# Kernel optimization log

Measured on AMD Instinct MI355X. Metric: run time of the kernel, lower is better.

The kernel has to match this reference:

```python
import jax, jax.numpy as jnp
import numpy as np

N_NODES = 50000
N_EDGES = 800000
NUM_FEAT = 100
F_DIM = 64
R_ROUNDS = 4
L_FP = 128
NUM_CLASS = 10


def setup_inputs() -> dict:
    key = jax.random.key(0)
    ks = jax.random.split(key, 10)
    s = 0.05
    return {
        "node_feature": jax.random.randint(ks[0], (N_NODES,), 0, NUM_FEAT),
        "edge_src": jax.random.randint(ks[1], (N_EDGES,), 0, N_NODES),
        "edge_dst": jax.random.randint(ks[2], (N_EDGES,), 0, N_NODES),
        "emb_table": jax.random.normal(ks[3], (NUM_FEAT, F_DIM), jnp.float32) * s,
        "W_h": jax.random.normal(ks[4], (R_ROUNDS, F_DIM, F_DIM), jnp.float32) * s,
        "b_h": jax.random.normal(ks[5], (R_ROUNDS, F_DIM), jnp.float32) * s,
        "W_fp": jax.random.normal(ks[6], (R_ROUNDS, F_DIM, L_FP), jnp.float32) * s,
        "b_fp": jax.random.normal(ks[7], (R_ROUNDS, L_FP), jnp.float32) * s,
        "W_cl": jax.random.normal(ks[8], (L_FP, NUM_CLASS), jnp.float32) * s,
        "b_cl": jax.random.normal(ks[9], (NUM_CLASS,), jnp.float32) * s,
    }


def reference(node_feature, edge_src, edge_dst, emb_table, W_h, b_h, W_fp, b_fp, W_cl, b_cl):
    # Initial node embeddings: [N, F]
    emb = emb_table[node_feature]
    f = jnp.zeros((L_FP,), dtype=emb.dtype)
    for r_i in range(R_ROUNDS):
        # v[node] = emb[node] + sum_{nbr in neighbours(node)} emb[nbr]
        agg = jax.ops.segment_sum(emb[edge_src], edge_dst, num_segments=N_NODES)
        v = emb + agg
        # per-node tiny MLP, batched over all nodes
        r = jax.nn.relu(v @ W_h[r_i] + b_h[r_i])            # [N, F]
        i = jax.nn.softmax(r @ W_fp[r_i] + b_fp[r_i], axis=-1)  # [N, L]
        f = f + i.sum(axis=0)                                # accumulate fingerprint
        emb = r                                              # synchronous update
    return jax.nn.softmax(f @ W_cl + b_cl, axis=-1)
```

## Files before the change

### kernel.cpp

```cpp
#include <hip/hip_runtime.h>
#include <hip/hip_bf16.h>

#define FDIM 64
#define LFP 128
#define RROUNDS 4
#define BM 64
#define PCHUNK 4096
#define CB 512
#define MAXB 10240
#define RSL 32

typedef __attribute__((ext_vector_type(8))) short bf16x8;
typedef __attribute__((ext_vector_type(4))) float f32x4;

__device__ __forceinline__ float bf2f(unsigned short u) {
    unsigned int x = ((unsigned int)u) << 16;
    float f;
    __builtin_memcpy(&f, &x, 4);
    return f;
}
__device__ __forceinline__ unsigned short f2bf(float x) {
    unsigned int u;
    __builtin_memcpy(&u, &x, 4);
    unsigned int r = (u + 0x7fffu + ((u >> 16) & 1u)) >> 16;
    return (unsigned short)r;
}

__global__ __launch_bounds__(256) void chist_kernel(const int* __restrict__ dst,
                                                    int* __restrict__ chist, int nE, int nbc) {
    __shared__ int scnt[128];
    int t = threadIdx.x;
    if (t < 128) scnt[t] = 0;
    __syncthreads();
    int c0 = blockIdx.x * PCHUNK;
#pragma unroll
    for (int k = 0; k < PCHUNK / 256; ++k) {
        int idx = c0 + k * 256 + t;
        if (idx < nE) atomicAdd(&scnt[dst[idx] >> 9], 1);
    }
    __syncthreads();
    if (t < nbc && scnt[t] > 0) atomicAdd(&chist[t], scnt[t]);
}

__global__ __launch_bounds__(128) void cscan_kernel(const int* __restrict__ chist,
                                                    int* __restrict__ cbase,
                                                    int* __restrict__ ccursor, int nbc, int nE) {
    __shared__ int s[128];
    int t = threadIdx.x;
    int v = (t < nbc) ? chist[t] : 0;
    s[t] = v;
    __syncthreads();
    for (int d = 1; d < 128; d <<= 1) {
        int x = (t >= d) ? s[t - d] : 0;
        __syncthreads();
        s[t] += x;
        __syncthreads();
    }
    int ex = s[t] - v;
    if (t < nbc) { cbase[t] = ex; ccursor[t] = ex; }
    if (t == 0) cbase[nbc] = nE;
}

__global__ __launch_bounds__(256) void partition_kernel(
        const int* __restrict__ esrc, const int* __restrict__ edst,
        int* __restrict__ ccursor, int* __restrict__ tmp, int nE, int nbc) {
    __shared__ int scnt[128], sinc[128], sexc[128], sgbase[128], scur[128];
    __shared__ int sbuf[PCHUNK];
    __shared__ int starg[PCHUNK];
    int t = threadIdx.x;
    int c0 = blockIdx.x * PCHUNK;
    int cend = c0 + PCHUNK; if (cend > nE) cend = nE;

    if (t < 128) scnt[t] = 0;
    __syncthreads();
#pragma unroll
    for (int k = 0; k < PCHUNK / 256; ++k) {
        int idx = c0 + k * 256 + t;
        if (idx < cend) atomicAdd(&scnt[edst[idx] >> 9], 1);
    }
    __syncthreads();
    if (t < 128) sinc[t] = scnt[t];
    __syncthreads();
    for (int d = 1; d < 128; d <<= 1) {
        int x = (t >= d && t < 128) ? sinc[t - d] : 0;
        __syncthreads();
        if (t < 128) sinc[t] += x;
        __syncthreads();
    }
    if (t < 128) {
        int ex = sinc[t] - scnt[t];
        sexc[t] = ex;
        scur[t] = ex;
        sgbase[t] = (t < nbc && scnt[t] > 0) ? atomicAdd(&ccursor[t], scnt[t]) : 0;
    }
    __syncthreads();
#pragma unroll
    for (int k = 0; k < PCHUNK / 256; ++k) {
        int idx = c0 + k * 256 + t;
        if (idx < cend) {
            int s = esrc[idx], d = edst[idx];
            int b = d >> 9;
            int pos = atomicAdd(&scur[b], 1);
            sbuf[pos] = (s << 9) | (d & 511);
            starg[pos] = sgbase[b] + (pos - sexc[b]);
        }
    }
    __syncthreads();
    int cnt = cend - c0;
#pragma unroll
    for (int k = 0; k < PCHUNK / 256; ++k) {
        int li = k * 256 + t;
        if (li < cnt) tmp[starg[li]] = sbuf[li];
    }
}

__global__ __launch_bounds__(256) void bsort_kernel(
        const int* __restrict__ cbase, const int* __restrict__ tmp,
        unsigned short* __restrict__ csr16, int* __restrict__ rp, int N, int nE) {
    __shared__ unsigned short ssrc[MAXB];
    __shared__ int pcnt[CB], pexc[CB], pcur[CB];
    __shared__ int ssum[256];
    int t = threadIdx.x;
    int b = blockIdx.x;
    int lo = cbase[b], hi = cbase[b + 1];

    pcnt[t] = 0; pcnt[t + 256] = 0;
    __syncthreads();
    for (int idx = lo + t; idx < hi; idx += 256)
        atomicAdd(&pcnt[tmp[idx] & 511], 1);
    __syncthreads();
    int a0 = pcnt[2 * t], a1 = pcnt[2 * t + 1];
    ssum[t] = a0 + a1;
    __syncthreads();
    for (int d = 1; d < 256; d <<= 1) {
        int x = (t >= d) ? ssum[t - d] : 0;
        __syncthreads();
        ssum[t] += x;
        __syncthreads();
    }
    int ex = ssum[t] - (a0 + a1);
    pexc[2 * t] = ex;          pcur[2 * t] = ex;
    pexc[2 * t + 1] = ex + a0; pcur[2 * t + 1] = ex + a0;
    __syncthreads();
#pragma unroll
    for (int i = t; i < CB; i += 256) {
        int node = b * CB + i;
        if (node < N) rp[node] = lo + pexc[i];
    }
    if (b == 0 && t == 0) rp[N] = nE;
    for (int idx = lo + t; idx < hi; idx += 256) {
        int e = tmp[idx];
        int pos = atomicAdd(&pcur[e & 511], 1);
        ssrc[pos] = (unsigned short)(e >> 9);
    }
    __syncthreads();
    int cnt = hi - lo;
    for (int li = t; li < cnt; li += 256) csr16[lo + li] = ssrc[li];
}

__global__ void prep_kernel(const float* __restrict__ Wh, const float* __restrict__ Wfp,
                            unsigned short* __restrict__ whT, unsigned short* __restrict__ wfpT) {
    int o = blockIdx.x * blockDim.x + threadIdx.x;
    if (o < RROUNDS * FDIM * FDIM) {
        int r = o >> 12, rem = o & 4095, j = rem >> 6, k = rem & 63;
        whT[o] = f2bf(Wh[r * 4096 + k * 64 + j]);
    } else {
        int o2 = o - RROUNDS * FDIM * FDIM;
        int r = o2 >> 13, rem = o2 & 8191, l = rem >> 6, k = rem & 63;
        wfpT[o2] = f2bf(Wfp[r * 8192 + k * 128 + l]);
    }
}

__global__ void init_kernel(const int* __restrict__ feat, const float* __restrict__ table,
                            unsigned short* __restrict__ emb, int n) {
    int gid = blockIdx.x * blockDim.x + threadIdx.x;
    if (gid < n * FDIM) {
        int node = gid >> 6;
        int d = gid & 63;
        emb[gid] = f2bf(table[feat[node] * FDIM + d]);
    }
}

__global__ __launch_bounds__(256) void gather_kernel(
        const unsigned short* __restrict__ emb, const int* __restrict__ rp,
        const unsigned short* __restrict__ csr16, unsigned short* __restrict__ vbuf, int N) {
    int wid = (int)((blockIdx.x * 256 + threadIdx.x) >> 6);
    int lane = threadIdx.x & 63;
    if (wid >= N) return;
    int start = rp[wid], end = rp[wid + 1];
    int grp = lane >> 3, q = lane & 7;
    float acc[8] = {0.f, 0.f, 0.f, 0.f, 0.f, 0.f, 0.f, 0.f};
    for (int j = start + grp; j < end; j += 8) {
        int nb = csr16[j];
        bf16x8 u = *reinterpret_cast<const bf16x8*>(emb + (size_t)nb * 64 + q * 8);
#pragma unroll
        for (int x = 0; x < 8; ++x) acc[x] += bf2f((unsigned short)u[x]);
    }
#pragma unroll
    for (int x = 0; x < 8; ++x) {
        acc[x] += __shfl_xor(acc[x], 8);
        acc[x] += __shfl_xor(acc[x], 16);
        acc[x] += __shfl_xor(acc[x], 32);
    }
    if (grp == 0) {
        bf16x8 self = *reinterpret_cast<const bf16x8*>(emb + (size_t)wid * 64 + q * 8);
        bf16x8 o;
#pragma unroll
        for (int x = 0; x < 8; ++x) o[x] = (short)f2bf(acc[x] + bf2f((unsigned short)self[x]));
        *reinterpret_cast<bf16x8*>(vbuf + (size_t)wid * 64 + q * 8) = o;
    }
}

__global__ __launch_bounds__(256) void mlp_kernel(
        const unsigned short* __restrict__ vbuf, unsigned short* __restrict__ emb_out,
        const unsigned short* __restrict__ whT, const unsigned short* __restrict__ wfpT,
        const float* __restrict__ bh, const float* __restrict__ bfp,
        float* __restrict__ fpart, int N) {
    __shared__ unsigned short sR[BM * 72];
    __shared__ float sFp[4][128];

    int tid = threadIdx.x;
    int base = blockIdx.x * BM;
    int lane = tid & 63, w = tid >> 6;
    int m16 = lane & 15, g = lane >> 4;
    int arow = w * 16 + m16;

    const unsigned short* vrow = vbuf + (size_t)(base + arow) * 64;
    bf16x8 a0 = *reinterpret_cast<const bf16x8*>(vrow + g * 8);
    bf16x8 a1 = *reinterpret_cast<const bf16x8*>(vrow + 32 + g * 8);

    f32x4 acc[4];
#pragma unroll
    for (int c = 0; c < 4; ++c) {
        bf16x8 b0 = *reinterpret_cast<const bf16x8*>(whT + (c * 16 + m16) * 64 + g * 8);
        bf16x8 b1 = *reinterpret_cast<const bf16x8*>(whT + (c * 16 + m16) * 64 + 32 + g * 8);
        f32x4 z = {0.f, 0.f, 0.f, 0.f};
        z = __builtin_amdgcn_mfma_f32_16x16x32_bf16(a0, b0, z, 0, 0, 0);
        z = __builtin_amdgcn_mfma_f32_16x16x32_bf16(a1, b1, z, 0, 0, 0);
        acc[c] = z;
    }
#pragma unroll
    for (int c = 0; c < 4; ++c) {
        float bias = bh[c * 16 + m16];
#pragma unroll
        for (int reg = 0; reg < 4; ++reg) {
            float rv = fmaxf(acc[c][reg] + bias, 0.f);
            sR[(w * 16 + g * 4 + reg) * 72 + c * 16 + m16] = f2bf(rv);
        }
    }

    bf16x8 ra0 = *reinterpret_cast<const bf16x8*>(sR + arow * 72 + g * 8);
    bf16x8 ra1 = *reinterpret_cast<const bf16x8*>(sR + arow * 72 + 32 + g * 8);

#pragma unroll
    for (int it = 0; it < 2; ++it) {
        int lidx = w * 1024 + it * 512 + lane * 8;
        int row = lidx >> 6;
        if (base + row < N)
            *reinterpret_cast<bf16x8*>(emb_out + (size_t)base * 64 + lidx) =
                *reinterpret_cast<const bf16x8*>(sR + row * 72 + (lidx & 63));
    }

    f32x4 z[8];
#pragma unroll
    for (int t = 0; t < 8; ++t) {
        bf16x8 b0 = *reinterpret_cast<const bf16x8*>(wfpT + (t * 16 + m16) * 64 + g * 8);
        bf16x8 b1 = *reinterpret_cast<const bf16x8*>(wfpT + (t * 16 + m16) * 64 + 32 + g * 8);
        f32x4 zz = {0.f, 0.f, 0.f, 0.f};
        zz = __builtin_amdgcn_mfma_f32_16x16x32_bf16(ra0, b0, zz, 0, 0, 0);
        zz = __builtin_amdgcn_mfma_f32_16x16x32_bf16(ra1, b1, zz, 0, 0, 0);
        float bias = bfp[t * 16 + m16];
#pragma unroll
        for (int reg = 0; reg < 4; ++reg) zz[reg] += bias;
        z[t] = zz;
    }

#pragma unroll
    for (int reg = 0; reg < 4; ++reg) {
        float mx = -1e30f;
#pragma unroll
        for (int t = 0; t < 8; ++t) mx = fmaxf(mx, z[t][reg]);
#pragma unroll
        for (int d = 1; d < 16; d <<= 1) mx = fmaxf(mx, __shfl_xor(mx, d));
        float s = 0.f;
#pragma unroll
        for (int t = 0; t < 8; ++t) {
            float p = __expf(z[t][reg] - mx);
            z[t][reg] = p;
            s += p;
        }
#pragma unroll
        for (int d = 1; d < 16; d <<= 1) s += __shfl_xor(s, d);
        int node = base + w * 16 + g * 4 + reg;
        float inv = (node < N) ? (1.f / s) : 0.f;
#pragma unroll
        for (int t = 0; t < 8; ++t) z[t][reg] *= inv;
    }
#pragma unroll
    for (int t = 0; t < 8; ++t) {
        float v = z[t][0] + z[t][1] + z[t][2] + z[t][3];
        v += __shfl_xor(v, 16);
        v += __shfl_xor(v, 32);
        if (g == 0) sFp[w][t * 16 + m16] = v;
    }
    __syncthreads();
    if (tid < 128) {
        float s = sFp[0][tid] + sFp[1][tid] + sFp[2][tid] + sFp[3][tid];
        fpart[(size_t)blockIdx.x * 128 + tid] = s;
    }
}

__global__ __launch_bounds__(256) void reduce1_kernel(const float* __restrict__ fpart,
                                                      float* __restrict__ fred, int nslice) {
    __shared__ float sAcc[128];
    int t = threadIdx.x;
    int col = t & 127, gp = t >> 7;
    int base = blockIdx.x * RSL + gp * (RSL / 2);
    const float* p = fpart + (size_t)base * 128 + col;
    float a0 = 0.f, a1 = 0.f, a2 = 0.f, a3 = 0.f;
    if (base + RSL / 2 <= nslice) {
#pragma unroll
        for (int k = 0; k < 4; ++k) {
            a0 += p[(k * 4 + 0) * 128];
            a1 += p[(k * 4 + 1) * 128];
            a2 += p[(k * 4 + 2) * 128];
            a3 += p[(k * 4 + 3) * 128];
        }
    } else {
        int cnt = nslice - base; if (cnt < 0) cnt = 0;
        for (int k = 0; k < cnt; ++k) a0 += p[k * 128];
    }
    float s = (a0 + a1) + (a2 + a3);
    if (gp == 1) sAcc[col] = s;
    __syncthreads();
    if (gp == 0) fred[(size_t)blockIdx.x * 128 + col] = s + sAcc[col];
}

__global__ __launch_bounds__(256) void final_kernel(const float* __restrict__ fred, int nred,
                                                    const float* __restrict__ Wcl,
                                                    const float* __restrict__ bcl,
                                                    float* __restrict__ out) {
    __shared__ float sAcc[128];
    __shared__ float sf[128];
    __shared__ float logits[10];
    int t = threadIdx.x;
    int col = t & 127, gp = t >> 7;
    int half = (nred + 1) >> 1;
    int b0 = gp * half;
    int b1 = b0 + half; if (b1 > nred) b1 = nred;
    float a0 = 0.f, a1 = 0.f, a2 = 0.f, a3 = 0.f;
    const float* p = fred + col;
    int b = b0;
    for (; b + 4 <= b1; b += 4) {
        a0 += p[(size_t)(b + 0) * 128];
        a1 += p[(size_t)(b + 1) * 128];
        a2 += p[(size_t)(b + 2) * 128];
        a3 += p[(size_t)(b + 3) * 128];
    }
    for (; b < b1; ++b) a0 += p[(size_t)b * 128];
    float s = (a0 + a1) + (a2 + a3);
    if (gp == 1) sAcc[col] = s;
    __syncthreads();
    if (gp == 0) sf[col] = s + sAcc[col];
    __syncthreads();
    if (t < 10) {
        float acc = bcl[t];
        for (int l = 0; l < LFP; l++) acc = fmaf(sf[l], Wcl[l * 10 + t], acc);
        logits[t] = acc;
    }
    __syncthreads();
    if (t == 0) {
        float m = -1e30f;
        for (int i = 0; i < 10; i++) m = fmaxf(m, logits[i]);
        float e[10], s2 = 0.f;
        for (int i = 0; i < 10; i++) { e[i] = __expf(logits[i] - m); s2 += e[i]; }
        for (int i = 0; i < 10; i++) out[i] = e[i] / s2;
    }
}

extern "C" void kernel_launch(void* const* d_in, const int* in_sizes, int n_in,
                              void* d_out, int out_size, void* d_ws, size_t ws_size,
                              hipStream_t stream) {
    const int* feat = (const int*)d_in[0];
    const int* esrc = (const int*)d_in[1];
    const int* edst = (const int*)d_in[2];
    const float* table = (const float*)d_in[3];
    const float* Wh = (const float*)d_in[4];
    const float* bh = (const float*)d_in[5];
    const float* Wfp = (const float*)d_in[6];
    const float* bfp = (const float*)d_in[7];
    const float* Wcl = (const float*)d_in[8];
    const float* bcl = (const float*)d_in[9];
    float* out = (float*)d_out;
    int N = in_sizes[0];
    int nE = in_sizes[1];

    int nbm = (N + BM - 1) / BM;
    int nbc = (N + CB - 1) / CB;
    int nbp = (nE + PCHUNK - 1) / PCHUNK;
    int nslice = RROUNDS * nbm;
    int nred = (nslice + RSL - 1) / RSL;

    char* ws = (char*)d_ws;
    size_t off = 0;
    auto alloc = [&](size_t bytes) { void* p = ws + off; off += (bytes + 63) & ~(size_t)63; return p; };
    unsigned short* embA = (unsigned short*)alloc((size_t)N * 64 * 2);
    unsigned short* vbuf = (unsigned short*)alloc((size_t)(N + BM) * 64 * 2);
    unsigned short* whT  = (unsigned short*)alloc(RROUNDS * 64 * 64 * 2);
    unsigned short* wfpT = (unsigned short*)alloc(RROUNDS * 128 * 64 * 2);
    float* fpart = (float*)alloc((size_t)nslice * 128 * 4);
    float* fred  = (float*)alloc((size_t)nred * 128 * 4);
    int* chist   = (int*)alloc(128 * 4);
    int* cbase   = (int*)alloc(129 * 4);
    int* ccursor = (int*)alloc(128 * 4);
    int* rp      = (int*)alloc(((size_t)N + 1) * 4);
    int* tmp     = (int*)alloc((size_t)nE * 4);
    unsigned short* csr16 = (unsigned short*)alloc((size_t)nE * 2);

    hipMemsetAsync(chist, 0, 128 * 4, stream);
    chist_kernel<<<nbp, 256, 0, stream>>>(edst, chist, nE, nbc);
    cscan_kernel<<<1, 128, 0, stream>>>(chist, cbase, ccursor, nbc, nE);
    partition_kernel<<<nbp, 256, 0, stream>>>(esrc, edst, ccursor, tmp, nE, nbc);
    bsort_kernel<<<nbc, 256, 0, stream>>>(cbase, tmp, csr16, rp, N, nE);

    prep_kernel<<<192, 256, 0, stream>>>(Wh, Wfp, whT, wfpT);
    init_kernel<<<(N * FDIM + 255) / 256, 256, 0, stream>>>(feat, table, embA, N);

    for (int r = 0; r < RROUNDS; ++r) {
        gather_kernel<<<(N * 64 + 255) / 256, 256, 0, stream>>>(embA, rp, csr16, vbuf, N);
        mlp_kernel<<<nbm, 256, 0, stream>>>(
            vbuf, embA, whT + (size_t)r * 4096, wfpT + (size_t)r * 8192,
            bh + (size_t)r * FDIM, bfp + (size_t)r * LFP,
            fpart + (size_t)r * nbm * 128, N);
    }

    reduce1_kernel<<<nred, 256, 0, stream>>>(fpart, fred, nslice);
    final_kernel<<<1, 256, 0, stream>>>(fred, nred, Wcl, bcl, out);
}
```

Baseline: 252.7 us.

## Fuse neighbour gather into per-round MLP kernel with fixed-point LDS atomics

Merges the gather and MLP kernels into one per-round kernel. Each 64-node block walks its CSR edge range and accumulates neighbour embeddings into shared memory using integer atomics on fixed-point scaled values, then adds the self term and runs the MFMA MLP. Embeddings are ping-ponged between two buffers, and the prep and init kernels are merged into one setup kernel. This removes the vbuf round trip and one launch per round, at the cost of 32-bit CSR entries, per-element LDS atomics, one 2-byte load per lane per edge instead of vector loads, and fixed-point quantization of the sums.

```diff
diff --git a/kernel.cpp b/kernel.cpp
--- a/kernel.cpp
+++ b/kernel.cpp
@@ -9,6 +9,8 @@
 #define CB 512
 #define MAXB 10240
 #define RSL 32
+#define SCALE 16777216.0f
+#define INV_SCALE 5.9604644775390625e-8f
 
 typedef __attribute__((ext_vector_type(8))) short bf16x8;
 typedef __attribute__((ext_vector_type(4))) float f32x4;
@@ -116,8 +118,8 @@
 
 __global__ __launch_bounds__(256) void bsort_kernel(
         const int* __restrict__ cbase, const int* __restrict__ tmp,
-        unsigned short* __restrict__ csr16, int* __restrict__ rp, int N, int nE) {
-    __shared__ unsigned short ssrc[MAXB];
+        int* __restrict__ csr32, int* __restrict__ rp, int N, int nE) {
+    __shared__ int sdat[MAXB];
     __shared__ int pcnt[CB], pexc[CB], pcur[CB];
     __shared__ int ssum[256];
     int t = threadIdx.x;
@@ -151,83 +153,83 @@
     for (int idx = lo + t; idx < hi; idx += 256) {
         int e = tmp[idx];
         int pos = atomicAdd(&pcur[e & 511], 1);
-        ssrc[pos] = (unsigned short)(e >> 9);
+        sdat[pos] = e;
     }
     __syncthreads();
     int cnt = hi - lo;
-    for (int li = t; li < cnt; li += 256) csr16[lo + li] = ssrc[li];
-}
-
-__global__ void prep_kernel(const float* __restrict__ Wh, const float* __restrict__ Wfp,
-                            unsigned short* __restrict__ whT, unsigned short* __restrict__ wfpT) {
-    int o = blockIdx.x * blockDim.x + threadIdx.x;
-    if (o < RROUNDS * FDIM * FDIM) {
-        int r = o >> 12, rem = o & 4095, j = rem >> 6, k = rem & 63;
-        whT[o] = f2bf(Wh[r * 4096 + k * 64 + j]);
-    } else {
-        int o2 = o - RROUNDS * FDIM * FDIM;
+    for (int li = t; li < cnt; li += 256) csr32[lo + li] = sdat[li];
+}
+
+__global__ void setup_kernel(const int* __restrict__ feat, const float* __restrict__ table,
+                             const float* __restrict__ Wh, const float* __restrict__ Wfp,
+                             unsigned short* __restrict__ emb, unsigned short* __restrict__ whT,
+                             unsigned short* __restrict__ wfpT, int n) {
+    int gid = blockIdx.x * blockDim.x + threadIdx.x;
+    if (gid < RROUNDS * FDIM * FDIM) {
+        int r = gid >> 12, rem = gid & 4095, j = rem >> 6, k = rem & 63;
+        whT[gid] = f2bf(Wh[r * 4096 + k * 64 + j]);
+    } else if (gid < RROUNDS * FDIM * FDIM + RROUNDS * LFP * FDIM) {
+        int o2 = gid - RROUNDS * FDIM * FDIM;
         int r = o2 >> 13, rem = o2 & 8191, l = rem >> 6, k = rem & 63;
         wfpT[o2] = f2bf(Wfp[r * 8192 + k * 128 + l]);
     }
-}
-
-__global__ void init_kernel(const int* __restrict__ feat, const float* __restrict__ table,
-                            unsigned short* __restrict__ emb, int n) {
-    int gid = blockIdx.x * blockDim.x + threadIdx.x;
-    if (gid < n * FDIM) {
-        int node = gid >> 6;
-        int d = gid & 63;
-        emb[gid] = f2bf(table[feat[node] * FDIM + d]);
-    }
-}
-
-__global__ __launch_bounds__(256) void gather_kernel(
-        const unsigned short* __restrict__ emb, const int* __restrict__ rp,
-        const unsigned short* __restrict__ csr16, unsigned short* __restrict__ vbuf, int N) {
-    int wid = (int)((blockIdx.x * 256 + threadIdx.x) >> 6);
-    int lane = threadIdx.x & 63;
-    if (wid >= N) return;
-    int start = rp[wid], end = rp[wid + 1];
-    int grp = lane >> 3, q = lane & 7;
-    float acc[8] = {0.f, 0.f, 0.f, 0.f, 0.f, 0.f, 0.f, 0.f};
-    for (int j = start + grp; j < end; j += 8) {
-        int nb = csr16[j];
-        bf16x8 u = *reinterpret_cast<const bf16x8*>(emb + (size_t)nb * 64 + q * 8);
-#pragma unroll
-        for (int x = 0; x < 8; ++x) acc[x] += bf2f((unsigned short)u[x]);
-    }
-#pragma unroll
-    for (int x = 0; x < 8; ++x) {
-        acc[x] += __shfl_xor(acc[x], 8);
-        acc[x] += __shfl_xor(acc[x], 16);
-        acc[x] += __shfl_xor(acc[x], 32);
-    }
-    if (grp == 0) {
-        bf16x8 self = *reinterpret_cast<const bf16x8*>(emb + (size_t)wid * 64 + q * 8);
-        bf16x8 o;
-#pragma unroll
-        for (int x = 0; x < 8; ++x) o[x] = (short)f2bf(acc[x] + bf2f((unsigned short)self[x]));
-        *reinterpret_cast<bf16x8*>(vbuf + (size_t)wid * 64 + q * 8) = o;
-    }
-}
-
-__global__ __launch_bounds__(256) void mlp_kernel(
-        const unsigned short* __restrict__ vbuf, unsigned short* __restrict__ emb_out,
+    if (gid < n * FDIM)
+        emb[gid] = f2bf(table[feat[gid >> 6] * FDIM + (gid & 63)]);
+}
+
+__global__ __launch_bounds__(256) void round_kernel(
+        const unsigned short* __restrict__ embIn, unsigned short* __restrict__ embOut,
+        const int* __restrict__ rp, const int* __restrict__ csr32,
         const unsigned short* __restrict__ whT, const unsigned short* __restrict__ wfpT,
         const float* __restrict__ bh, const float* __restrict__ bfp,
         float* __restrict__ fpart, int N) {
+    __shared__ int sAcc[BM * 68];
     __shared__ unsigned short sR[BM * 72];
     __shared__ float sFp[4][128];
 
     int tid = threadIdx.x;
     int base = blockIdx.x * BM;
     int lane = tid & 63, w = tid >> 6;
+
+    for (int i = tid; i < BM * 68; i += 256) sAcc[i] = 0;
+    __syncthreads();
+
+    {
+        int hiNode = base + BM; if (hiNode > N) hiNode = N;
+        int pStart = rp[base], pEnd = rp[hiNode];
+        int dbase = (blockIdx.x & 7) << 6;
+#pragma unroll 4
+        for (int p = pStart + w; p < pEnd; p += 4) {
+            int e = csr32[p];
+            int src = e >> 9;
+            int dl = (e & 511) - dbase;
+            float v = bf2f(embIn[(size_t)src * 64 + lane]);
+            atomicAdd(&sAcc[dl * 68 + lane], __float2int_rn(v * SCALE));
+        }
+    }
+    __syncthreads();
+
     int m16 = lane & 15, g = lane >> 4;
     int arow = w * 16 + m16;
-
-    const unsigned short* vrow = vbuf + (size_t)(base + arow) * 64;
-    bf16x8 a0 = *reinterpret_cast<const bf16x8*>(vrow + g * 8);
-    bf16x8 a1 = *reinterpret_cast<const bf16x8*>(vrow + 32 + g * 8);
+    int node = base + arow;
+
+    bf16x8 a0, a1;
+    {
+        const int* ar = sAcc + arow * 68;
+        if (node < N) {
+            const unsigned short* sp = embIn + (size_t)node * 64;
+            bf16x8 s0 = *reinterpret_cast<const bf16x8*>(sp + g * 8);
+            bf16x8 s1 = *reinterpret_cast<const bf16x8*>(sp + 32 + g * 8);
+#pragma unroll
+            for (int x = 0; x < 8; ++x) {
+                a0[x] = (short)f2bf((float)ar[g * 8 + x] * INV_SCALE + bf2f((unsigned short)s0[x]));
+                a1[x] = (short)f2bf((float)ar[32 + g * 8 + x] * INV_SCALE + bf2f((unsigned short)s1[x]));
+            }
+        } else {
+#pragma unroll
+            for (int x = 0; x < 8; ++x) { a0[x] = 0; a1[x] = 0; }
+        }
+    }
 
     f32x4 acc[4];
 #pragma unroll
@@ -257,7 +259,7 @@
         int lidx = w * 1024 + it * 512 + lane * 8;
         int row = lidx >> 6;
         if (base + row < N)
-            *reinterpret_cast<bf16x8*>(emb_out + (size_t)base * 64 + lidx) =
+            *reinterpret_cast<bf16x8*>(embOut + (size_t)base * 64 + lidx) =
                 *reinterpret_cast<const bf16x8*>(sR + row * 72 + (lidx & 63));
     }
 
@@ -291,8 +293,8 @@
         }
 #pragma unroll
         for (int d = 1; d < 16; d <<= 1) s += __shfl_xor(s, d);
-        int node = base + w * 16 + g * 4 + reg;
-        float inv = (node < N) ? (1.f / s) : 0.f;
+        int nd = base + w * 16 + g * 4 + reg;
+        float inv = (nd < N) ? (1.f / s) : 0.f;
 #pragma unroll
         for (int t = 0; t < 8; ++t) z[t][reg] *= inv;
     }
@@ -405,7 +407,7 @@
     size_t off = 0;
     auto alloc = [&](size_t bytes) { void* p = ws + off; off += (bytes + 63) & ~(size_t)63; return p; };
     unsigned short* embA = (unsigned short*)alloc((size_t)N * 64 * 2);
-    unsigned short* vbuf = (unsigned short*)alloc((size_t)(N + BM) * 64 * 2);
+    unsigned short* embB = (unsigned short*)alloc((size_t)N * 64 * 2);
     unsigned short* whT  = (unsigned short*)alloc(RROUNDS * 64 * 64 * 2);
     unsigned short* wfpT = (unsigned short*)alloc(RROUNDS * 128 * 64 * 2);
     float* fpart = (float*)alloc((size_t)nslice * 128 * 4);
@@ -415,23 +417,24 @@
     int* ccursor = (int*)alloc(128 * 4);
     int* rp      = (int*)alloc(((size_t)N + 1) * 4);
     int* tmp     = (int*)alloc((size_t)nE * 4);
-    unsigned short* csr16 = (unsigned short*)alloc((size_t)nE * 2);
+    int* csr32   = (int*)alloc((size_t)nE * 4);
 
     hipMemsetAsync(chist, 0, 128 * 4, stream);
     chist_kernel<<<nbp, 256, 0, stream>>>(edst, chist, nE, nbc);
     cscan_kernel<<<1, 128, 0, stream>>>(chist, cbase, ccursor, nbc, nE);
     partition_kernel<<<nbp, 256, 0, stream>>>(esrc, edst, ccursor, tmp, nE, nbc);
-    bsort_kernel<<<nbc, 256, 0, stream>>>(cbase, tmp, csr16, rp, N, nE);
-
-    prep_kernel<<<192, 256, 0, stream>>>(Wh, Wfp, whT, wfpT);
-    init_kernel<<<(N * FDIM + 255) / 256, 256, 0, stream>>>(feat, table, embA, N);
-
+    bsort_kernel<<<nbc, 256, 0, stream>>>(cbase, tmp, csr32, rp, N, nE);
+
+    setup_kernel<<<(N * FDIM + 255) / 256, 256, 0, stream>>>(feat, table, Wh, Wfp, embA, whT, wfpT, N);
+
+    unsigned short* eIn = embA;
+    unsigned short* eOut = embB;
     for (int r = 0; r < RROUNDS; ++r) {
-        gather_kernel<<<(N * 64 + 255) / 256, 256, 0, stream>>>(embA, rp, csr16, vbuf, N);
-        mlp_kernel<<<nbm, 256, 0, stream>>>(
-            vbuf, embA, whT + (size_t)r * 4096, wfpT + (size_t)r * 8192,
+        round_kernel<<<nbm, 256, 0, stream>>>(
+            eIn, eOut, rp, csr32, whT + (size_t)r * 4096, wfpT + (size_t)r * 8192,
             bh + (size_t)r * FDIM, bfp + (size_t)r * LFP,
             fpart + (size_t)r * nbm * 128, N);
+        unsigned short* t = eIn; eIn = eOut; eOut = t;
     }
 
     reduce1_kernel<<<nred, 256, 0, stream>>>(fpart, fred, nslice);
```

Measured after the change: 652.3 us. +158.1%, slower.

## Drop histogram pass by partitioning into fixed-capacity buckets and merge setup kernels

Applied to the files above, without the earlier changes.

Removes the separate destination-histogram and scan kernels and the memset. The partition kernel now writes each coarse bucket into a fixed MAXB-sized slot, and the bucket sort computes bucket offsets itself with an in-block prefix scan over the atomic counts. The weight-transpose, embedding-init and counter-zeroing work is fused into a single setup kernel, cutting the launch count and one full read of edge_dst. The cost is a larger tmp buffer, and correctness now depends on no bucket exceeding MAXB edges, which holds for these uniform random inputs but is not guaranteed in general.

```diff
diff --git a/kernel.cpp b/kernel.cpp
--- a/kernel.cpp
+++ b/kernel.cpp
@@ -26,44 +26,28 @@
     return (unsigned short)r;
 }
 
-__global__ __launch_bounds__(256) void chist_kernel(const int* __restrict__ dst,
-                                                    int* __restrict__ chist, int nE, int nbc) {
-    __shared__ int scnt[128];
-    int t = threadIdx.x;
-    if (t < 128) scnt[t] = 0;
-    __syncthreads();
-    int c0 = blockIdx.x * PCHUNK;
-#pragma unroll
-    for (int k = 0; k < PCHUNK / 256; ++k) {
-        int idx = c0 + k * 256 + t;
-        if (idx < nE) atomicAdd(&scnt[dst[idx] >> 9], 1);
-    }
-    __syncthreads();
-    if (t < nbc && scnt[t] > 0) atomicAdd(&chist[t], scnt[t]);
-}
-
-__global__ __launch_bounds__(128) void cscan_kernel(const int* __restrict__ chist,
-                                                    int* __restrict__ cbase,
-                                                    int* __restrict__ ccursor, int nbc, int nE) {
-    __shared__ int s[128];
-    int t = threadIdx.x;
-    int v = (t < nbc) ? chist[t] : 0;
-    s[t] = v;
-    __syncthreads();
-    for (int d = 1; d < 128; d <<= 1) {
-        int x = (t >= d) ? s[t - d] : 0;
-        __syncthreads();
-        s[t] += x;
-        __syncthreads();
-    }
-    int ex = s[t] - v;
-    if (t < nbc) { cbase[t] = ex; ccursor[t] = ex; }
-    if (t == 0) cbase[nbc] = nE;
+__global__ void setup_kernel(const int* __restrict__ feat, const float* __restrict__ table,
+                             const float* __restrict__ Wh, const float* __restrict__ Wfp,
+                             unsigned short* __restrict__ emb, unsigned short* __restrict__ whT,
+                             unsigned short* __restrict__ wfpT, int* __restrict__ bucketCount,
+                             int n) {
+    int gid = blockIdx.x * blockDim.x + threadIdx.x;
+    if (gid < RROUNDS * FDIM * FDIM) {
+        int r = gid >> 12, rem = gid & 4095, j = rem >> 6, k = rem & 63;
+        whT[gid] = f2bf(Wh[r * 4096 + k * 64 + j]);
+    } else if (gid < RROUNDS * FDIM * FDIM + RROUNDS * LFP * FDIM) {
+        int o2 = gid - RROUNDS * FDIM * FDIM;
+        int r = o2 >> 13, rem = o2 & 8191, l = rem >> 6, k = rem & 63;
+        wfpT[o2] = f2bf(Wfp[r * 8192 + k * 128 + l]);
+    }
+    if (gid < n * FDIM)
+        emb[gid] = f2bf(table[feat[gid >> 6] * FDIM + (gid & 63)]);
+    if (gid < 128) bucketCount[gid] = 0;
 }
 
 __global__ __launch_bounds__(256) void partition_kernel(
         const int* __restrict__ esrc, const int* __restrict__ edst,
-        int* __restrict__ ccursor, int* __restrict__ tmp, int nE, int nbc) {
+        int* __restrict__ bucketCount, int* __restrict__ tmp, int nE, int nbc) {
     __shared__ int scnt[128], sinc[128], sexc[128], sgbase[128], scur[128];
     __shared__ int sbuf[PCHUNK];
     __shared__ int starg[PCHUNK];
@@ -91,7 +75,8 @@
         int ex = sinc[t] - scnt[t];
         sexc[t] = ex;
         scur[t] = ex;
-        sgbase[t] = (t < nbc && scnt[t] > 0) ? atomicAdd(&ccursor[t], scnt[t]) : 0;
+        sgbase[t] = (t < nbc && scnt[t] > 0)
+                        ? t * MAXB + atomicAdd(&bucketCount[t], scnt[t]) : 0;
     }
     __syncthreads();
 #pragma unroll
@@ -115,19 +100,31 @@
 }
 
 __global__ __launch_bounds__(256) void bsort_kernel(
-        const int* __restrict__ cbase, const int* __restrict__ tmp,
-        unsigned short* __restrict__ csr16, int* __restrict__ rp, int N, int nE) {
+        const int* __restrict__ bucketCount, const int* __restrict__ tmp,
+        unsigned short* __restrict__ csr16, int* __restrict__ rp, int N, int nE, int nbc) {
     __shared__ unsigned short ssrc[MAXB];
     __shared__ int pcnt[CB], pexc[CB], pcur[CB];
     __shared__ int ssum[256];
+    __shared__ int sS[128];
     int t = threadIdx.x;
     int b = blockIdx.x;
-    int lo = cbase[b], hi = cbase[b + 1];
+
+    if (t < 128) sS[t] = (t < nbc) ? bucketCount[t] : 0;
+    __syncthreads();
+    for (int d = 1; d < 128; d <<= 1) {
+        int x = (t >= d && t < 128) ? sS[t - d] : 0;
+        __syncthreads();
+        if (t < 128) sS[t] += x;
+        __syncthreads();
+    }
+    int lo = (b == 0) ? 0 : sS[b - 1];
+    int cnt = sS[b] - lo;
 
     pcnt[t] = 0; pcnt[t + 256] = 0;
     __syncthreads();
-    for (int idx = lo + t; idx < hi; idx += 256)
-        atomicAdd(&pcnt[tmp[idx] & 511], 1);
+    const int* bt = tmp + (size_t)b * MAXB;
+    for (int idx = t; idx < cnt; idx += 256)
+        atomicAdd(&pcnt[bt[idx] & 511], 1);
     __syncthreads();
     int a0 = pcnt[2 * t], a1 = pcnt[2 * t + 1];
     ssum[t] = a0 + a1;
@@ -148,37 +145,13 @@
         if (node < N) rp[node] = lo + pexc[i];
     }
     if (b == 0 && t == 0) rp[N] = nE;
-    for (int idx = lo + t; idx < hi; idx += 256) {
-        int e = tmp[idx];
+    for (int idx = t; idx < cnt; idx += 256) {
+        int e = bt[idx];
         int pos = atomicAdd(&pcur[e & 511], 1);
         ssrc[pos] = (unsigned short)(e >> 9);
     }
     __syncthreads();
-    int cnt = hi - lo;
     for (int li = t; li < cnt; li += 256) csr16[lo + li] = ssrc[li];
-}
-
-__global__ void prep_kernel(const float* __restrict__ Wh, const float* __restrict__ Wfp,
-                            unsigned short* __restrict__ whT, unsigned short* __restrict__ wfpT) {
-    int o = blockIdx.x * blockDim.x + threadIdx.x;
-    if (o < RROUNDS * FDIM * FDIM) {
-        int r = o >> 12, rem = o & 4095, j = rem >> 6, k = rem & 63;
-        whT[o] = f2bf(Wh[r * 4096 + k * 64 + j]);
-    } else {
-        int o2 = o - RROUNDS * FDIM * FDIM;
-        int r = o2 >> 13, rem = o2 & 8191, l = rem >> 6, k = rem & 63;
-        wfpT[o2] = f2bf(Wfp[r * 8192 + k * 128 + l]);
-    }
-}
-
-__global__ void init_kernel(const int* __restrict__ feat, const float* __restrict__ table,
-                            unsigned short* __restrict__ emb, int n) {
-    int gid = blockIdx.x * blockDim.x + threadIdx.x;
-    if (gid < n * FDIM) {
-        int node = gid >> 6;
-        int d = gid & 63;
-        emb[gid] = f2bf(table[feat[node] * FDIM + d]);
-    }
 }
 
 __global__ __launch_bounds__(256) void gather_kernel(
@@ -410,21 +383,16 @@
     unsigned short* wfpT = (unsigned short*)alloc(RROUNDS * 128 * 64 * 2);
     float* fpart = (float*)alloc((size_t)nslice * 128 * 4);
     float* fred  = (float*)alloc((size_t)nred * 128 * 4);
-    int* chist   = (int*)alloc(128 * 4);
-    int* cbase   = (int*)alloc(129 * 4);
-    int* ccursor = (int*)alloc(128 * 4);
+    int* bucketCount = (int*)alloc(128 * 4);
     int* rp      = (int*)alloc(((size_t)N + 1) * 4);
-    int* tmp     = (int*)alloc((size_t)nE * 4);
+    int* tmp     = (int*)alloc((size_t)nbc * MAXB * 4);
     unsigned short* csr16 = (unsigned short*)alloc((size_t)nE * 2);
 
-    hipMemsetAsync(chist, 0, 128 * 4, stream);
-    chist_kernel<<<nbp, 256, 0, stream>>>(edst, chist, nE, nbc);
-    cscan_kernel<<<1, 128, 0, stream>>>(chist, cbase, ccursor, nbc, nE);
-    partition_kernel<<<nbp, 256, 0, stream>>>(esrc, edst, ccursor, tmp, nE, nbc);
-    bsort_kernel<<<nbc, 256, 0, stream>>>(cbase, tmp, csr16, rp, N, nE);
-
-    prep_kernel<<<192, 256, 0, stream>>>(Wh, Wfp, whT, wfpT);
-    init_kernel<<<(N * FDIM + 255) / 256, 256, 0, stream>>>(feat, table, embA, N);
+    setup_kernel<<<(N * FDIM + 255) / 256, 256, 0, stream>>>(
+        feat, table, Wh, Wfp, embA, whT, wfpT, bucketCount, N);
+
+    partition_kernel<<<nbp, 256, 0, stream>>>(esrc, edst, bucketCount, tmp, nE, nbc);
+    bsort_kernel<<<nbc, 256, 0, stream>>>(bucketCount, tmp, csr16, rp, N, nE, nbc);
 
     for (int r = 0; r < RROUNDS; ++r) {
         gather_kernel<<<(N * 64 + 255) / 256, 256, 0, stream>>>(embA, rp, csr16, vbuf, N);
```

New measurement: 238.9 us. 1.06x faster.
